# Optimization experiments

Hardware: AMD Instinct MI355X
Metric: run time of the kernel (lower is better)

The kernel has to match this reference:

```python
import jax, jax.numpy as jnp
from jax import lax
import numpy as np

B, L_IN, L_OUT, N, COV = 16, 96, 24, 320, 4
E, H = 64, 128
CIN = E + COV


def setup_inputs() -> dict:
    key = jax.random.key(0)
    ks = jax.random.split(key, 16)
    s = 0.05
    inp = {
        'history_data': jax.random.normal(ks[0], (B, L_IN, N, 1 + COV), jnp.float32),
        'future_data': jax.random.normal(ks[1], (B, L_OUT, N, 1 + COV), jnp.float32),
        'We': jax.random.normal(ks[2], (E, 1), jnp.float32) * s,
        'be': jnp.zeros((E,), jnp.float32),
        'Wih0': jax.random.normal(ks[3], (4 * H, CIN), jnp.float32) * s,
        'Whh0': jax.random.normal(ks[4], (4 * H, H), jnp.float32) * s,
        'bih0': jnp.zeros((4 * H,), jnp.float32),
        'bhh0': jnp.zeros((4 * H,), jnp.float32),
        'Wih1': jax.random.normal(ks[5], (4 * H, H), jnp.float32) * s,
        'Whh1': jax.random.normal(ks[6], (4 * H, H), jnp.float32) * s,
        'bih1': jnp.zeros((4 * H,), jnp.float32),
        'bhh1': jnp.zeros((4 * H,), jnp.float32),
        'Wh': jax.random.normal(ks[7], (2, H), jnp.float32) * s,
        'bh': jnp.zeros((2,), jnp.float32),
        'train': 1,
    }
    return inp


def _run_layer(xs, Wih, Whh, bih, bhh):
    # xs: [T, BN, Cin] -> ys: [T, BN, H]
    h0 = jnp.zeros((xs.shape[1], Whh.shape[1]), xs.dtype)

    def step(carry, x):
        h, c = carry
        g = x @ Wih.T + bih + h @ Whh.T + bhh  # [BN, 4H]
        i, f, gg, o = jnp.split(g, 4, axis=-1)  # torch gate order i,f,g,o
        c = jax.nn.sigmoid(f) * c + jax.nn.sigmoid(i) * jnp.tanh(gg)
        h = jax.nn.sigmoid(o) * jnp.tanh(c)
        return (h, c), h

    (_, _), ys = lax.scan(step, (h0, h0), xs)
    return ys


def reference(history_data, future_data, We, be, Wih0, Whh0, bih0, bhh0,
              Wih1, Whh1, bih1, bhh1, Wh, bh, train):
    # train branch (teacher forcing): history_next is always ground truth
    T = L_IN + L_OUT
    tgt = jnp.concatenate([history_data[..., 0:1], future_data[..., 0:1]], axis=1)  # [B,T,N,1]
    cov = jnp.concatenate([history_data[..., 1:], future_data[..., 1:]], axis=1)   # [B,T,N,COV]
    # step t uses target at t-1 and covariates at t, for t = 1..T-1
    embed = tgt[:, :T - 1] @ We.T + be                       # [B,T-1,N,E]
    enc_in = jnp.concatenate([embed, cov[:, 1:T]], axis=-1)  # [B,T-1,N,CIN]
    xs = enc_in.transpose(1, 0, 2, 3).reshape(T - 1, B * N, CIN)
    ys = _run_layer(xs, Wih0, Whh0, bih0, bhh0)
    ys = _run_layer(ys, Wih1, Whh1, bih1, bhh1)
    hid = jax.nn.relu(ys)                                    # [T-1, BN, H]
    head = hid @ Wh.T + bh                                   # [T-1, BN, 2]
    mu = head[..., 0:1]
    sigma = jax.nn.softplus(head[..., 1:2])
    p = jnp.concatenate([mu, sigma], axis=-1)
    p = p[-L_OUT:].reshape(L_OUT, B, N, 2).transpose(1, 0, 2, 3)  # [B,L_out,N,2]
    return p
```

## Files before the change

kernel.cpp:

```cpp
#include <hip/hip_runtime.h>

typedef __bf16 bf16x8 __attribute__((ext_vector_type(8)));
typedef unsigned short us8 __attribute__((ext_vector_type(8)));
typedef float f32x4 __attribute__((ext_vector_type(4)));

#define NROW 32
#define A_STR 136
#define NSTEP 119

__device__ __forceinline__ unsigned short f2bf(float f){
  unsigned int x = __builtin_bit_cast(unsigned int, f);
  x += 0x7fffu + ((x >> 16) & 1u);
  return (unsigned short)(x >> 16);
}
__device__ __forceinline__ float bf2f(unsigned short s){
  unsigned int x = ((unsigned int)s) << 16;
  return __builtin_bit_cast(float, x);
}
__device__ __forceinline__ float sigm(float x){ return 1.0f/(1.0f + __expf(-x)); }
__device__ __forceinline__ float tanh_(float x){ float e = __expf(2.0f*x); return 1.0f - 2.0f/(e + 1.0f); }

__device__ __forceinline__ f32x4 MFMA(us8 a, us8 b, f32x4 c){
  return __builtin_amdgcn_mfma_f32_16x16x32_bf16(
      __builtin_bit_cast(bf16x8, a), __builtin_bit_cast(bf16x8, b), c, 0, 0, 0);
}

__device__ __forceinline__ void mfma_ag_first(f32x4& d, us8 a, us8 b){
  asm("s_nop 1\n\tv_mfma_f32_16x16x32_bf16 %0, %1, %2, %0" : "+v"(d) : "v"(a), "a"(b));
}
__device__ __forceinline__ void mfma_ag(f32x4& d, us8 a, us8 b){
  asm("v_mfma_f32_16x16x32_bf16 %0, %1, %2, %0" : "+v"(d) : "v"(a), "a"(b));
}
__device__ __forceinline__ void accfence8(f32x4& a0, f32x4& a1, f32x4& a2, f32x4& a3,
                                          f32x4& a4, f32x4& a5, f32x4& a6, f32x4& a7){
  asm("s_nop 7\n\ts_nop 7\n\ts_nop 2"
      : "+v"(a0), "+v"(a1), "+v"(a2), "+v"(a3),
        "+v"(a4), "+v"(a5), "+v"(a6), "+v"(a7));
}

struct SharedMem {
  unsigned short A0[2][NROW*A_STR];
  unsigned short A1[2][NROW*A_STR];
  unsigned short Ax[2][NROW][32];
  unsigned short xw[512*8];
  float c_lds[2][2][2][256][4];
  float b1[512];
  float Wh2f[256];
  float red[NROW][8][2];
  float we_s[64];
  float be_s[64];
  float bh_s[2];
};

__global__ __launch_bounds__(256)
__attribute__((amdgpu_waves_per_eu(1, 1)))
void deepar_kernel(
    const float* __restrict__ hist, const float* __restrict__ fut,
    const float* __restrict__ We,   const float* __restrict__ be,
    const float* __restrict__ Wih0, const float* __restrict__ Whh0,
    const float* __restrict__ bih0, const float* __restrict__ bhh0,
    const float* __restrict__ Wih1, const float* __restrict__ Whh1,
    const float* __restrict__ bih1, const float* __restrict__ bhh1,
    const float* __restrict__ Wh,   const float* __restrict__ bh,
    float* __restrict__ out)
{
  __shared__ SharedMem S;
  const int tid = threadIdx.x;
  const int wg  = blockIdx.x;
  const int b   = wg / 10;
  const int n0  = (wg % 10) * NROW;
  const int w   = tid >> 6;
  const int l   = tid & 63;
  const int gq  = l >> 4;
  const int r   = l & 15;
  const int hbase = w * 32;

  {
    us8 z = {0,0,0,0,0,0,0,0};
    us8* pA0 = (us8*)&S.A0[0][0];
    us8* pA1 = (us8*)&S.A1[0][0];
    for (int i = tid; i < 2*NROW*A_STR/8; i += 256){ pA0[i] = z; pA1[i] = z; }
    ((us8*)&S.Ax[0][0][0])[tid] = z;
    f32x4 zf = {0.f,0.f,0.f,0.f};
    #pragma unroll
    for (int q = 0; q < 8; ++q) *(f32x4*)&S.c_lds[q >> 2][(q >> 1) & 1][q & 1][tid][0] = zf;
  }
  S.Wh2f[tid] = Wh[tid];
  if (tid < 64)       S.we_s[tid]       = We[tid];
  else if (tid < 128) S.be_s[tid - 64]  = be[tid - 64];
  else if (tid < 130) S.bh_s[tid - 128] = bh[tid - 128];
  __syncthreads();

  for (int cc = tid; cc < 512; cc += 256){
    const float* wr = Wih0 + cc * 68;
    float u = 0.f, v = 0.f;
    #pragma unroll 8
    for (int e = 0; e < 64; ++e){
      float wv = wr[e];
      u = fmaf(wv, S.we_s[e], u);
      v = fmaf(wv, S.be_s[e], v);
    }
    v += bih0[cc] + bhh0[cc];
    unsigned short* xp = &S.xw[cc * 8];
    xp[0] = f2bf(u);
    xp[1] = f2bf(wr[64]); xp[2] = f2bf(wr[65]); xp[3] = f2bf(wr[66]); xp[4] = f2bf(wr[67]);
    xp[5] = f2bf(v);
    xp[6] = 0; xp[7] = 0;
    S.b1[cc] = bih1[cc] + bhh1[cc];
  }
  if (tid < 64){ int row = tid >> 1, bsel = tid & 1; S.Ax[bsel][row][5] = 0x3F80; }
  if (tid < 160){
    int srow, sch, tau;
    if (tid < 32){ srow = tid; sch = 0; tau = 0; }
    else { int k = tid - 32; srow = k >> 2; sch = 1 + (k & 3); tau = 1; }
    const float* p = hist + ((b*96 + tau)*320 + n0 + srow)*5;
    S.Ax[0][srow][sch] = f2bf(p[sch]);
  }

  us8 WV[4][2][4], WA1[4][2][4], WA2[4][2][4];
  #pragma unroll
  for (int m = 0; m < 3; ++m){
    const float* base = (m == 0) ? Whh0 : (m == 1) ? Wih1 : Whh1;
    #pragma unroll
    for (int g = 0; g < 4; ++g){
      #pragma unroll
      for (int ct = 0; ct < 2; ++ct){
        int col = g*128 + hbase + ct*16 + r;
        #pragma unroll
        for (int q = 0; q < 4; ++q){
          const float* p = base + col*128 + q*32 + gq*8;
          f32x4 x0 = *(const f32x4*)p;
          f32x4 x1 = *(const f32x4*)(p + 4);
          us8 tt;
          tt[0]=f2bf(x0[0]); tt[1]=f2bf(x0[1]); tt[2]=f2bf(x0[2]); tt[3]=f2bf(x0[3]);
          tt[4]=f2bf(x1[0]); tt[5]=f2bf(x1[1]); tt[6]=f2bf(x1[2]); tt[7]=f2bf(x1[3]);
          if (m == 0) WV[g][ct][q]  = tt;
          else if (m == 1) WA1[g][ct][q] = tt;
          else WA2[g][ct][q] = tt;
        }
      }
    }
  }

  __syncthreads();

  for (int t = 0; t < NSTEP; ++t){
    const int pb = t & 1, nb = pb ^ 1;
    const unsigned short* A0r = S.A0[pb];
    unsigned short*       A0w = S.A0[nb];
    const unsigned short* A1r = S.A1[pb];
    unsigned short*       A1w = S.A1[nb];

    float stv = 0.f; int sto = -1;
    if (t + 1 < NSTEP && tid < 160){
      int srow, sch, tau;
      if (tid < 32){ srow = tid; sch = 0; tau = t + 1; }
      else { int k = tid - 32; srow = k >> 2; sch = 1 + (k & 3); tau = t + 2; }
      const float* p = (tau < 96) ? (hist + ((b*96 + tau)*320 + n0 + srow)*5)
                                  : (fut  + ((b*24 + (tau - 96))*320 + n0 + srow)*5);
      stv = p[sch];
      sto = nb*NROW*32 + srow*32 + sch;
    }

    #pragma unroll
    for (int rt = 0; rt < 2; ++rt){
      const int rbase = rt * 16;
      f32x4 acc[4][2];
      us8 ax = *(const us8*)&S.Ax[pb][rbase + r][gq*8];
      #pragma unroll
      for (int g = 0; g < 4; ++g)
        #pragma unroll
        for (int ct = 0; ct < 2; ++ct){
          us8 bx = *(const us8*)&S.xw[(g*128 + hbase + ct*16 + r)*8];
          f32x4 z = {0.f,0.f,0.f,0.f};
          acc[g][ct] = MFMA(ax, bx, z);
        }
      #pragma unroll
      for (int q = 0; q < 4; ++q){
        us8 a = *(const us8*)&A0r[(rbase + r)*A_STR + q*32 + gq*8];
        #pragma unroll
        for (int g = 0; g < 4; ++g)
          #pragma unroll
          for (int ct = 0; ct < 2; ++ct)
            acc[g][ct] = MFMA(a, WV[g][ct][q], acc[g][ct]);
      }
      f32x4 cpr[2], cn[2];
      cpr[0] = *(const f32x4*)&S.c_lds[0][rt][0][tid][0];
      cpr[1] = *(const f32x4*)&S.c_lds[0][rt][1][tid][0];
      #pragma unroll
      for (int ct = 0; ct < 2; ++ct)
        #pragma unroll
        for (int j = 0; j < 4; ++j){
          float c = fmaf(sigm(acc[1][ct][j]), cpr[ct][j],
                         sigm(acc[0][ct][j]) * tanh_(acc[2][ct][j]));
          cn[ct][j] = c;
          float h = sigm(acc[3][ct][j]) * tanh_(c);
          A0w[(rbase + gq*4 + j)*A_STR + hbase + ct*16 + r] = f2bf(h);
        }
      *(f32x4*)&S.c_lds[0][rt][0][tid][0] = cn[0];
      *(f32x4*)&S.c_lds[0][rt][1][tid][0] = cn[1];
    }
    __syncthreads();

    #pragma unroll
    for (int rt = 0; rt < 2; ++rt){
      const int rbase = rt * 16;
      f32x4 acc[4][2];
      #pragma unroll
      for (int g = 0; g < 4; ++g)
        #pragma unroll
        for (int ct = 0; ct < 2; ++ct){
          float bv = S.b1[g*128 + hbase + ct*16 + r];
          f32x4 iv = {bv, bv, bv, bv};
          acc[g][ct] = iv;
        }
      {
        us8 a = *(const us8*)&A0w[(rbase + r)*A_STR + 0*32 + gq*8];
        #pragma unroll
        for (int g = 0; g < 4; ++g)
          #pragma unroll
          for (int ct = 0; ct < 2; ++ct)
            mfma_ag_first(acc[g][ct], a, WA1[g][ct][0]);
      }
      #pragma unroll
      for (int q = 1; q < 4; ++q){
        us8 a = *(const us8*)&A0w[(rbase + r)*A_STR + q*32 + gq*8];
        #pragma unroll
        for (int g = 0; g < 4; ++g)
          #pragma unroll
          for (int ct = 0; ct < 2; ++ct)
            mfma_ag(acc[g][ct], a, WA1[g][ct][q]);
      }
      #pragma unroll
      for (int q = 0; q < 4; ++q){
        us8 a = *(const us8*)&A1r[(rbase + r)*A_STR + q*32 + gq*8];
        #pragma unroll
        for (int g = 0; g < 4; ++g)
          #pragma unroll
          for (int ct = 0; ct < 2; ++ct)
            mfma_ag(acc[g][ct], a, WA2[g][ct][q]);
      }
      accfence8(acc[0][0], acc[0][1], acc[1][0], acc[1][1],
                acc[2][0], acc[2][1], acc[3][0], acc[3][1]);
      f32x4 cpr[2], cn[2];
      cpr[0] = *(const f32x4*)&S.c_lds[1][rt][0][tid][0];
      cpr[1] = *(const f32x4*)&S.c_lds[1][rt][1][tid][0];
      #pragma unroll
      for (int ct = 0; ct < 2; ++ct)
        #pragma unroll
        for (int j = 0; j < 4; ++j){
          float c = fmaf(sigm(acc[1][ct][j]), cpr[ct][j],
                         sigm(acc[0][ct][j]) * tanh_(acc[2][ct][j]));
          cn[ct][j] = c;
          float h = sigm(acc[3][ct][j]) * tanh_(c);
          A1w[(rbase + gq*4 + j)*A_STR + hbase + ct*16 + r] = f2bf(h);
        }
      *(f32x4*)&S.c_lds[1][rt][0][tid][0] = cn[0];
      *(f32x4*)&S.c_lds[1][rt][1][tid][0] = cn[1];
    }
    if (sto >= 0) ((unsigned short*)&S.Ax[0][0][0])[sto] = f2bf(stv);
    __syncthreads();

    if (t >= 95){
      const int rown = tid >> 3, cg = tid & 7;
      us8 hv0 = *(const us8*)&A1w[rown*A_STR + cg*16];
      us8 hv1 = *(const us8*)&A1w[rown*A_STR + cg*16 + 8];
      float pm = 0.f, ps = 0.f;
      #pragma unroll
      for (int k = 0; k < 8; ++k){
        float ha = bf2f(hv0[k]); ha = ha > 0.f ? ha : 0.f;
        float hb = bf2f(hv1[k]); hb = hb > 0.f ? hb : 0.f;
        pm = fmaf(ha, S.Wh2f[cg*16 + k], pm);
        pm = fmaf(hb, S.Wh2f[cg*16 + 8 + k], pm);
        ps = fmaf(ha, S.Wh2f[128 + cg*16 + k], ps);
        ps = fmaf(hb, S.Wh2f[128 + cg*16 + 8 + k], ps);
      }
      S.red[rown][cg][0] = pm; S.red[rown][cg][1] = ps;
      __syncthreads();
      if (tid < 64){
        int row = tid >> 1, o = tid & 1;
        float s = S.bh_s[o];
        #pragma unroll
        for (int k = 0; k < 8; ++k) s += S.red[row][k][o];
        if (o) s = (s > 15.f) ? s : __logf(1.0f + __expf(s));
        out[((b*24 + (t - 95))*320 + (n0 + row))*2 + o] = s;
      }
    }
  }
}

extern "C" void kernel_launch(void* const* d_in, const int* in_sizes, int n_in,
                              void* d_out, int out_size, void* d_ws, size_t ws_size,
                              hipStream_t stream) {
  const float* hist = (const float*)d_in[0];
  const float* fut  = (const float*)d_in[1];
  const float* We   = (const float*)d_in[2];
  const float* be   = (const float*)d_in[3];
  const float* Wih0 = (const float*)d_in[4];
  const float* Whh0 = (const float*)d_in[5];
  const float* bih0 = (const float*)d_in[6];
  const float* bhh0 = (const float*)d_in[7];
  const float* Wih1 = (const float*)d_in[8];
  const float* Whh1 = (const float*)d_in[9];
  const float* bih1 = (const float*)d_in[10];
  const float* bhh1 = (const float*)d_in[11];
  const float* Wh   = (const float*)d_in[12];
  const float* bh   = (const float*)d_in[13];
  float* out = (float*)d_out;

  deepar_kernel<<<dim3(160), dim3(256), 0, stream>>>(
      hist, fut, We, be, Wih0, Whh0, bih0, bhh0,
      Wih1, Whh1, bih1, bhh1, Wh, bh, out);
}
```

Measured before the change: 1.109 ms.

## Move half of layer-0 recurrent weights to LDS and reorder layer-1 MFMAs

Half of the Whh0 bf16 fragments (the first two K-chunks) now live in a padded LDS array and are read each step, no longer held in registers. This frees VGPR/AGPR pressure, which is already tight with three full weight sets held per wave. Layer 1 now starts its accumulation with the q=3 chunk of the previous-step hidden state, which needs no input from this step's layer-0 output. This lets the first MFMA issue without waiting on the fresh A0w reads and drops the s_nop-padded first instruction. The cost is extra LDS reads per step and more shared memory, with bank padding (strides 40 and 521) meant to limit conflicts.

```diff
diff --git a/kernel.cpp b/kernel.cpp
--- a/kernel.cpp
+++ b/kernel.cpp
@@ -6,6 +6,8 @@
 
 #define NROW 32
 #define A_STR 136
+#define AX_STR 40
+#define WL_STR 521
 #define NSTEP 119
 
 __device__ __forceinline__ unsigned short f2bf(float f){
@@ -23,10 +25,6 @@
 __device__ __forceinline__ f32x4 MFMA(us8 a, us8 b, f32x4 c){
   return __builtin_amdgcn_mfma_f32_16x16x32_bf16(
       __builtin_bit_cast(bf16x8, a), __builtin_bit_cast(bf16x8, b), c, 0, 0, 0);
-}
-
-__device__ __forceinline__ void mfma_ag_first(f32x4& d, us8 a, us8 b){
-  asm("s_nop 1\n\tv_mfma_f32_16x16x32_bf16 %0, %1, %2, %0" : "+v"(d) : "v"(a), "a"(b));
 }
 __device__ __forceinline__ void mfma_ag(f32x4& d, us8 a, us8 b){
   asm("v_mfma_f32_16x16x32_bf16 %0, %1, %2, %0" : "+v"(d) : "v"(a), "a"(b));
@@ -41,8 +39,9 @@
 struct SharedMem {
   unsigned short A0[2][NROW*A_STR];
   unsigned short A1[2][NROW*A_STR];
-  unsigned short Ax[2][NROW][32];
+  unsigned short Ax[2][NROW][AX_STR];
   unsigned short xw[512*8];
+  unsigned short W0l[8*WL_STR*8];
   float c_lds[2][2][2][256][4];
   float b1[512];
   float Wh2f[256];
@@ -80,7 +79,8 @@
     us8* pA0 = (us8*)&S.A0[0][0];
     us8* pA1 = (us8*)&S.A1[0][0];
     for (int i = tid; i < 2*NROW*A_STR/8; i += 256){ pA0[i] = z; pA1[i] = z; }
-    ((us8*)&S.Ax[0][0][0])[tid] = z;
+    us8* pAx = (us8*)&S.Ax[0][0][0];
+    for (int i = tid; i < 2*NROW*AX_STR/8; i += 256) pAx[i] = z;
     f32x4 zf = {0.f,0.f,0.f,0.f};
     #pragma unroll
     for (int q = 0; q < 8; ++q) *(f32x4*)&S.c_lds[q >> 2][(q >> 1) & 1][q & 1][tid][0] = zf;
@@ -108,6 +108,16 @@
     xp[6] = 0; xp[7] = 0;
     S.b1[cc] = bih1[cc] + bhh1[cc];
   }
+  for (int idx = tid; idx < 8*512; idx += 256){
+    int qgq = idx >> 9, col = idx & 511;
+    const float* p = Whh0 + col*128 + qgq*8;
+    f32x4 x0 = *(const f32x4*)p;
+    f32x4 x1 = *(const f32x4*)(p + 4);
+    us8 tt;
+    tt[0]=f2bf(x0[0]); tt[1]=f2bf(x0[1]); tt[2]=f2bf(x0[2]); tt[3]=f2bf(x0[3]);
+    tt[4]=f2bf(x1[0]); tt[5]=f2bf(x1[1]); tt[6]=f2bf(x1[2]); tt[7]=f2bf(x1[3]);
+    *(us8*)&S.W0l[(qgq*WL_STR + col)*8] = tt;
+  }
   if (tid < 64){ int row = tid >> 1, bsel = tid & 1; S.Ax[bsel][row][5] = 0x3F80; }
   if (tid < 160){
     int srow, sch, tau;
@@ -117,7 +127,7 @@
     S.Ax[0][srow][sch] = f2bf(p[sch]);
   }
 
-  us8 WV[4][2][4], WA1[4][2][4], WA2[4][2][4];
+  us8 WV[4][2][2], WV2[4][2], WA1[4][2][4], WA2[4][2][3];
   #pragma unroll
   for (int m = 0; m < 3; ++m){
     const float* base = (m == 0) ? Whh0 : (m == 1) ? Wih1 : Whh1;
@@ -128,15 +138,17 @@
         int col = g*128 + hbase + ct*16 + r;
         #pragma unroll
         for (int q = 0; q < 4; ++q){
+          if (m == 0 && q < 2) continue;
           const float* p = base + col*128 + q*32 + gq*8;
           f32x4 x0 = *(const f32x4*)p;
           f32x4 x1 = *(const f32x4*)(p + 4);
           us8 tt;
           tt[0]=f2bf(x0[0]); tt[1]=f2bf(x0[1]); tt[2]=f2bf(x0[2]); tt[3]=f2bf(x0[3]);
           tt[4]=f2bf(x1[0]); tt[5]=f2bf(x1[1]); tt[6]=f2bf(x1[2]); tt[7]=f2bf(x1[3]);
-          if (m == 0) WV[g][ct][q]  = tt;
-          else if (m == 1) WA1[g][ct][q] = tt;
-          else WA2[g][ct][q] = tt;
+          if (m == 0)            WV[g][ct][q-2] = tt;
+          else if (m == 1)       WA1[g][ct][q]  = tt;
+          else if (q < 3)        WA2[g][ct][q]  = tt;
+          else                   WV2[g][ct]     = tt;
         }
       }
     }
@@ -159,7 +171,7 @@
       const float* p = (tau < 96) ? (hist + ((b*96 + tau)*320 + n0 + srow)*5)
                                   : (fut  + ((b*24 + (tau - 96))*320 + n0 + srow)*5);
       stv = p[sch];
-      sto = nb*NROW*32 + srow*32 + sch;
+      sto = nb*NROW*AX_STR + srow*AX_STR + sch;
     }
 
     #pragma unroll
@@ -176,13 +188,24 @@
           acc[g][ct] = MFMA(ax, bx, z);
         }
       #pragma unroll
-      for (int q = 0; q < 4; ++q){
+      for (int q = 0; q < 2; ++q){
+        us8 a = *(const us8*)&A0r[(rbase + r)*A_STR + q*32 + gq*8];
+        #pragma unroll
+        for (int g = 0; g < 4; ++g)
+          #pragma unroll
+          for (int ct = 0; ct < 2; ++ct){
+            us8 bw = *(const us8*)&S.W0l[((q*4 + gq)*WL_STR + g*128 + hbase + ct*16 + r)*8];
+            acc[g][ct] = MFMA(a, bw, acc[g][ct]);
+          }
+      }
+      #pragma unroll
+      for (int q = 2; q < 4; ++q){
         us8 a = *(const us8*)&A0r[(rbase + r)*A_STR + q*32 + gq*8];
         #pragma unroll
         for (int g = 0; g < 4; ++g)
           #pragma unroll
           for (int ct = 0; ct < 2; ++ct)
-            acc[g][ct] = MFMA(a, WV[g][ct][q], acc[g][ct]);
+            acc[g][ct] = MFMA(a, WV[g][ct][q-2], acc[g][ct]);
       }
       f32x4 cpr[2], cn[2];
       cpr[0] = *(const f32x4*)&S.c_lds[0][rt][0][tid][0];
@@ -206,24 +229,17 @@
     for (int rt = 0; rt < 2; ++rt){
       const int rbase = rt * 16;
       f32x4 acc[4][2];
+      us8 a13 = *(const us8*)&A1r[(rbase + r)*A_STR + 3*32 + gq*8];
       #pragma unroll
       for (int g = 0; g < 4; ++g)
         #pragma unroll
         for (int ct = 0; ct < 2; ++ct){
           float bv = S.b1[g*128 + hbase + ct*16 + r];
           f32x4 iv = {bv, bv, bv, bv};
-          acc[g][ct] = iv;
-        }
-      {
-        us8 a = *(const us8*)&A0w[(rbase + r)*A_STR + 0*32 + gq*8];
-        #pragma unroll
-        for (int g = 0; g < 4; ++g)
-          #pragma unroll
-          for (int ct = 0; ct < 2; ++ct)
-            mfma_ag_first(acc[g][ct], a, WA1[g][ct][0]);
-      }
-      #pragma unroll
-      for (int q = 1; q < 4; ++q){
+          acc[g][ct] = MFMA(a13, WV2[g][ct], iv);
+        }
+      #pragma unroll
+      for (int q = 0; q < 4; ++q){
         us8 a = *(const us8*)&A0w[(rbase + r)*A_STR + q*32 + gq*8];
         #pragma unroll
         for (int g = 0; g < 4; ++g)
@@ -232,7 +248,7 @@
             mfma_ag(acc[g][ct], a, WA1[g][ct][q]);
       }
       #pragma unroll
-      for (int q = 0; q < 4; ++q){
+      for (int q = 0; q < 3; ++q){
         us8 a = *(const us8*)&A1r[(rbase + r)*A_STR + q*32 + gq*8];
         #pragma unroll
         for (int g = 0; g < 4; ++g)
```

Measured after the change: 1.269 ms. 1.14x slower.
